# Kernel tuning notes

Measured on AMD Instinct MI355X. Metric: run time of the kernel, lower is better.

Reference implementation:

```python
import jax, jax.numpy as jnp
import numpy as np

CE_WEIGHT = 1.0
TRIPLET_WEIGHT = 0.1
MARGIN = 0.2


def setup_inputs() -> dict:
    key = jax.random.key(0)
    k1, k2, k3 = jax.random.split(key, 3)
    B, D, V = 4096, 512, 6000
    logits = jax.random.normal(k1, (B, V), dtype=jnp.float32)
    embeddings = jax.random.normal(k2, (B, D), dtype=jnp.float32)
    labels = jax.random.randint(k3, (B,), 0, 512, dtype=jnp.int64)
    return {"logits": logits, "embeddings": embeddings, "labels": labels}


def _pairwise_dist(emb):
    # Euclidean cdist via gram matrix; safe sqrt (zero grad where d2 == 0).
    sq = jnp.sum(emb * emb, axis=-1)  # [B]
    d2 = sq[:, None] + sq[None, :] - 2.0 * (emb @ emb.T)  # [B, B]
    d2 = jnp.maximum(d2, 0.0)
    safe = jnp.where(d2 > 0.0, d2, 1.0)
    return jnp.where(d2 > 0.0, jnp.sqrt(safe), 0.0)


def _losses(logits, embeddings, labels):
    B = logits.shape[0]
    # Cross entropy (mean reduction, matching nn.CrossEntropyLoss).
    logp = jax.nn.log_softmax(logits, axis=-1)
    ce_loss = -jnp.mean(jnp.take_along_axis(logp, labels[:, None], axis=1)[:, 0])

    # Batch-hard triplet loss, fully vectorized (one masked amax/amin per row).
    dist = _pairwise_dist(embeddings)  # [B, B]
    same = labels[:, None] == labels[None, :]  # [B, B]
    eye = jnp.eye(B, dtype=bool)
    pos_mask = same & ~eye
    neg_mask = ~same
    neg_inf = jnp.float32(-np.inf)
    pos_inf = jnp.float32(np.inf)
    hardest_pos = jnp.max(jnp.where(pos_mask, dist, neg_inf), axis=1)  # [B]
    hardest_neg = jnp.min(jnp.where(neg_mask, dist, pos_inf), axis=1)  # [B]
    valid = jnp.any(pos_mask, axis=1) & jnp.any(neg_mask, axis=1)  # [B]
    per_row = jax.nn.relu(hardest_pos - hardest_neg + MARGIN)
    per_row = jnp.where(valid, per_row, 0.0)
    n_valid = jnp.sum(valid.astype(jnp.float32))
    triplet_loss = jnp.where(n_valid > 0, jnp.sum(per_row) / jnp.maximum(n_valid, 1.0), 0.0)

    total_loss = CE_WEIGHT * ce_loss + TRIPLET_WEIGHT * triplet_loss
    return total_loss, ce_loss, triplet_loss


def reference(logits, embeddings, labels):
    return _losses(logits, embeddings, labels)
```

## Files before the change

### kernel.cpp

```cpp
#include <hip/hip_runtime.h>
#include <hip/hip_bf16.h>
#include <math.h>

#define BN   4096
#define DN   512
#define VN   6000
#define NCLS 512

typedef __attribute__((ext_vector_type(8)))  short short8;
typedef __attribute__((ext_vector_type(16))) float f32x16;

__device__ __forceinline__ unsigned short f2bf(float x) {
  unsigned int u = __float_as_uint(x);
  u = (u + 0x7FFFu + ((u >> 16) & 1u)) >> 16;
  return (unsigned short)u;
}

__device__ __forceinline__ void gld_lds16(const unsigned short* g, unsigned short* l) {
  __builtin_amdgcn_global_load_lds(
      (const __attribute__((address_space(1))) void*)g,
      (__attribute__((address_space(3))) void*)l, 16, 0, 0);
}

__launch_bounds__(256)
__global__ void prep_kernel(const float* __restrict__ emb, const int* __restrict__ labels,
                            unsigned short* __restrict__ embh, float* __restrict__ sqn,
                            int* __restrict__ cnt, int* __restrict__ posb,
                            int* __restrict__ negb) {
  const int row  = blockIdx.x * 4 + (threadIdx.x >> 6);
  const int lane = threadIdx.x & 63;
  const float4* rp = (const float4*)(emb + (size_t)row * DN);
  float4 a = rp[lane];
  float4 b = rp[lane + 64];
  float ss = a.x * a.x + a.y * a.y + a.z * a.z + a.w * a.w
           + b.x * b.x + b.y * b.y + b.z * b.z + b.w * b.w;
  ushort4 ha, hb;
  ha.x = f2bf(a.x); ha.y = f2bf(a.y); ha.z = f2bf(a.z); ha.w = f2bf(a.w);
  hb.x = f2bf(b.x); hb.y = f2bf(b.y); hb.z = f2bf(b.z); hb.w = f2bf(b.w);
  ushort4* wp = (ushort4*)(embh + (size_t)row * DN);
  wp[lane] = ha;
  wp[lane + 64] = hb;
#pragma unroll
  for (int off = 1; off < 64; off <<= 1) ss += __shfl_xor(ss, off);
  if (lane == 0) {
    sqn[row] = ss;
    posb[row] = 0;
    negb[row] = 0x7F800000;
    atomicAdd(cnt + labels[row], 1);
  }
}

__launch_bounds__(256)
__global__ void ce_kernel(const float* __restrict__ logits,
                          const int* __restrict__ labels,
                          float* __restrict__ ce_part) {
  const int r0 = blockIdx.x * 2, r1 = r0 + 1;
  const int tid = threadIdx.x;
  const float* p0 = logits + (size_t)r0 * VN;
  const float* p1 = logits + (size_t)r1 * VN;
  const float x0 = p0[labels[r0]];
  const float x1 = p1[labels[r1]];
  const float4* q0 = (const float4*)p0;
  const float4* q1 = (const float4*)p1;
  float4 v0[6], v1[6];
#pragma unroll
  for (int u = 0; u < 6; ++u) {
    int j = tid + u * 256;
    if (j < VN / 4) { v0[u] = q0[j]; v1[u] = q1[j]; }
  }
  float s0 = 0.f, s1 = 0.f;
#pragma unroll
  for (int u = 0; u < 6; ++u) {
    int j = tid + u * 256;
    if (j < VN / 4) {
      s0 += __expf(v0[u].x) + __expf(v0[u].y) + __expf(v0[u].z) + __expf(v0[u].w);
      s1 += __expf(v1[u].x) + __expf(v1[u].y) + __expf(v1[u].z) + __expf(v1[u].w);
    }
  }
#pragma unroll
  for (int off = 1; off < 64; off <<= 1) {
    s0 += __shfl_xor(s0, off);
    s1 += __shfl_xor(s1, off);
  }
  __shared__ float sp0[4], sp1[4];
  if ((tid & 63) == 0) { sp0[tid >> 6] = s0; sp1[tid >> 6] = s1; }
  __syncthreads();
  if (tid == 0) {
    ce_part[r0] = logf(sp0[0] + sp0[1] + sp0[2] + sp0[3]) - x0;
    ce_part[r1] = logf(sp1[0] + sp1[1] + sp1[2] + sp1[3]) - x1;
  }
}

__launch_bounds__(64, 2)
__global__ void triplet_kernel(const unsigned short* __restrict__ embh,
                               const float* __restrict__ sqn,
                               const int* __restrict__ labels,
                               int* __restrict__ posb, int* __restrict__ negb) {
  __shared__ unsigned short sA[64 * 64];
  __shared__ unsigned short sB[64 * 64];

  const int lane = threadIdx.x;
  const int m = lane & 31;
  const int half = lane >> 5;

  const int t = blockIdx.x;
  int J = (int)((sqrtf(8.f * (float)t + 1.f) - 1.f) * 0.5f);
  while ((J + 1) * (J + 2) / 2 <= t) ++J;
  while (J * (J + 1) / 2 > t) --J;
  const int I = t - J * (J + 1) / 2;
  const int i0 = I * 64, j0 = J * 64;
  const bool diag = (I == J);

  const int lrow = lane >> 3;
  const int lchk = (lane & 7) ^ lrow;
  const unsigned short* gA = embh + (size_t)(i0 + lrow) * DN + lchk * 8;
  const unsigned short* gB = embh + (size_t)(j0 + lrow) * DN + lchk * 8;

  f32x16 acc[2][2] = {};
  f32x16 accT[2][2] = {};

  for (int ks = 0; ks < 8; ++ks) {
    const int kk = ks * 64;
    asm volatile("s_waitcnt lgkmcnt(0)" ::: "memory");
#pragma unroll
    for (int s = 0; s < 8; ++s)
      gld_lds16(gA + kk + (size_t)s * 8 * DN, &sA[s * 8 * 64]);
#pragma unroll
    for (int s = 0; s < 8; ++s)
      gld_lds16(gB + kk + (size_t)s * 8 * DN, &sB[s * 8 * 64]);
    asm volatile("s_waitcnt vmcnt(0)" ::: "memory");
#pragma unroll
    for (int q = 0; q < 4; ++q) {
      const int c = q * 2 + half;
      const int sw = ((c ^ (m & 7)) * 8);
      short8 a0 = *(const short8*)&sA[m * 64 + sw];
      short8 a1 = *(const short8*)&sA[(32 + m) * 64 + sw];
      short8 b0 = *(const short8*)&sB[m * 64 + sw];
      short8 b1 = *(const short8*)&sB[(32 + m) * 64 + sw];
      acc[0][0]  = __builtin_amdgcn_mfma_f32_32x32x16_bf16(a0, b0, acc[0][0], 0, 0, 0);
      acc[0][1]  = __builtin_amdgcn_mfma_f32_32x32x16_bf16(a0, b1, acc[0][1], 0, 0, 0);
      acc[1][0]  = __builtin_amdgcn_mfma_f32_32x32x16_bf16(a1, b0, acc[1][0], 0, 0, 0);
      acc[1][1]  = __builtin_amdgcn_mfma_f32_32x32x16_bf16(a1, b1, acc[1][1], 0, 0, 0);
      accT[0][0] = __builtin_amdgcn_mfma_f32_32x32x16_bf16(b0, a0, accT[0][0], 0, 0, 0);
      accT[0][1] = __builtin_amdgcn_mfma_f32_32x32x16_bf16(b0, a1, accT[0][1], 0, 0, 0);
      accT[1][0] = __builtin_amdgcn_mfma_f32_32x32x16_bf16(b1, a0, accT[1][0], 0, 0, 0);
      accT[1][1] = __builtin_amdgcn_mfma_f32_32x32x16_bf16(b1, a1, accT[1][1], 0, 0, 0);
    }
  }

  {
    const int gj0 = j0 + m, gj1 = j0 + 32 + m;
    const int cl0 = labels[gj0], cl1 = labels[gj1];
    const float cq0 = sqn[gj0], cq1 = sqn[gj1];
    float p0 = 0.f, p1 = 0.f, n0 = INFINITY, n1 = INFINITY;
#pragma unroll
    for (int rb = 0; rb < 2; ++rb) {
#pragma unroll
      for (int r = 0; r < 16; ++r) {
        const int gi = i0 + rb * 32 + (r & 3) + 8 * (r >> 2) + 4 * half;
        const int rl = labels[gi];
        const float rq = sqn[gi];
        const float d0 = fmaf(-2.f, acc[rb][0][r], rq + cq0);
        const float d1 = fmaf(-2.f, acc[rb][1][r], rq + cq1);
        if (rl == cl0) { if (gi != gj0) p0 = fmaxf(p0, d0); } else n0 = fminf(n0, d0);
        if (rl == cl1) { if (gi != gj1) p1 = fmaxf(p1, d1); } else n1 = fminf(n1, d1);
      }
    }
    p0 = fmaxf(p0, __shfl_xor(p0, 32)); n0 = fminf(n0, __shfl_xor(n0, 32));
    p1 = fmaxf(p1, __shfl_xor(p1, 32)); n1 = fminf(n1, __shfl_xor(n1, 32));
    if (half == 0) {
      atomicMax(posb + gj0, __float_as_int(p0));
      atomicMin(negb + gj0, __float_as_int(n0));
      atomicMax(posb + gj1, __float_as_int(p1));
      atomicMin(negb + gj1, __float_as_int(n1));
    }
  }

  if (!diag) {
    const int gj0 = i0 + m, gj1 = i0 + 32 + m;
    const int cl0 = labels[gj0], cl1 = labels[gj1];
    const float cq0 = sqn[gj0], cq1 = sqn[gj1];
    float p0 = 0.f, p1 = 0.f, n0 = INFINITY, n1 = INFINITY;
#pragma unroll
    for (int rb = 0; rb < 2; ++rb) {
#pragma unroll
      for (int r = 0; r < 16; ++r) {
        const int gi = j0 + rb * 32 + (r & 3) + 8 * (r >> 2) + 4 * half;
        const int rl = labels[gi];
        const float rq = sqn[gi];
        const float d0 = fmaf(-2.f, accT[rb][0][r], rq + cq0);
        const float d1 = fmaf(-2.f, accT[rb][1][r], rq + cq1);
        if (rl == cl0) p0 = fmaxf(p0, d0); else n0 = fminf(n0, d0);
        if (rl == cl1) p1 = fmaxf(p1, d1); else n1 = fminf(n1, d1);
      }
    }
    p0 = fmaxf(p0, __shfl_xor(p0, 32)); n0 = fminf(n0, __shfl_xor(n0, 32));
    p1 = fmaxf(p1, __shfl_xor(p1, 32)); n1 = fminf(n1, __shfl_xor(n1, 32));
    if (half == 0) {
      atomicMax(posb + gj0, __float_as_int(p0));
      atomicMin(negb + gj0, __float_as_int(n0));
      atomicMax(posb + gj1, __float_as_int(p1));
      atomicMin(negb + gj1, __float_as_int(n1));
    }
  }
}

__launch_bounds__(1024)
__global__ void finalize_kernel(const int* __restrict__ posb, const int* __restrict__ negb,
                                const int* __restrict__ labels, const int* __restrict__ cnt,
                                const float* __restrict__ ce_part, float* __restrict__ out) {
  const int tid = threadIdx.x;
  float cesum = 0.f, sum = 0.f, nv = 0.f;
#pragma unroll
  for (int u = 0; u < 4; ++u) {
    const int i = tid + u * 1024;
    cesum += ce_part[i];
    int c = cnt[labels[i]];
    float p = sqrtf(fmaxf(__int_as_float(posb[i]), 0.f));
    float n = sqrtf(fmaxf(__int_as_float(negb[i]), 0.f));
    float t = fmaxf(p - n + 0.2f, 0.f);
    if (c >= 2 && c < BN) { sum += t; nv += 1.f; }
  }
#pragma unroll
  for (int off = 1; off < 64; off <<= 1) {
    cesum += __shfl_xor(cesum, off);
    sum   += __shfl_xor(sum, off);
    nv    += __shfl_xor(nv, off);
  }
  __shared__ float s0[16], s1[16], s2[16];
  if ((tid & 63) == 0) { s0[tid >> 6] = cesum; s1[tid >> 6] = sum; s2[tid >> 6] = nv; }
  __syncthreads();
  if (tid == 0) {
    cesum = 0.f; sum = 0.f; nv = 0.f;
#pragma unroll
    for (int wv = 0; wv < 16; ++wv) { cesum += s0[wv]; sum += s1[wv]; nv += s2[wv]; }
    float trip = (nv > 0.f) ? sum / nv : 0.f;
    float ce = cesum * (1.f / BN);
    out[0] = ce + 0.1f * trip;
    out[1] = ce;
    out[2] = trip;
  }
}

extern "C" void kernel_launch(void* const* d_in, const int* in_sizes, int n_in,
                              void* d_out, int out_size, void* d_ws, size_t ws_size,
                              hipStream_t stream) {
  const float* logits = (const float*)d_in[0];
  const float* emb    = (const float*)d_in[1];
  const int*   labels = (const int*)d_in[2];
  float* out = (float*)d_out;

  char* ws = (char*)d_ws;
  unsigned short* embh = (unsigned short*)ws;
  float* sqn    = (float*)(ws + (size_t)BN * DN * 2);
  int*   posb   = (int*)((char*)sqn  + (size_t)BN * 4);
  int*   negb   = (int*)((char*)posb + (size_t)BN * 4);
  int*   cnt    = (int*)((char*)negb + (size_t)BN * 4);
  float* ce_part = (float*)((char*)cnt + (size_t)NCLS * 4);

  hipMemsetAsync(cnt, 0, (size_t)NCLS * 4, stream);
  hipLaunchKernelGGL(prep_kernel, dim3(BN / 4), dim3(256), 0, stream,
                     emb, labels, embh, sqn, cnt, posb, negb);
  hipLaunchKernelGGL(ce_kernel, dim3(BN / 2), dim3(256), 0, stream,
                     logits, labels, ce_part);
  hipLaunchKernelGGL(triplet_kernel, dim3(64 * 65 / 2), dim3(64), 0, stream,
                     embh, sqn, labels, posb, negb);
  hipLaunchKernelGGL(finalize_kernel, dim3(1), dim3(1024), 0, stream,
                     posb, negb, labels, cnt, ce_part, out);
}
```

Before: 193.4 us.

## Fuse cross-entropy and triplet tiles into one interleaved kernel launch

Merges the memory-bound cross-entropy row reduction and the compute-bound triplet MFMA tiles into one heterogeneous kernel. Blocks are interleaved so each triplet tile is followed by two single-row CE blocks, letting logits streaming overlap with matrix work on the same CUs. The first 32 blocks take the leftover triplet tiles. This drops one launch and the serialization between the two kernels, but CE now runs with 64-thread blocks holding 24 float4 registers each, which may raise register pressure and reduce occupancy.

```diff
diff --git a/kernel.cpp b/kernel.cpp
--- a/kernel.cpp
+++ b/kernel.cpp
@@ -50,60 +50,15 @@
   }
 }
 
-__launch_bounds__(256)
-__global__ void ce_kernel(const float* __restrict__ logits,
-                          const int* __restrict__ labels,
-                          float* __restrict__ ce_part) {
-  const int r0 = blockIdx.x * 2, r1 = r0 + 1;
-  const int tid = threadIdx.x;
-  const float* p0 = logits + (size_t)r0 * VN;
-  const float* p1 = logits + (size_t)r1 * VN;
-  const float x0 = p0[labels[r0]];
-  const float x1 = p1[labels[r1]];
-  const float4* q0 = (const float4*)p0;
-  const float4* q1 = (const float4*)p1;
-  float4 v0[6], v1[6];
-#pragma unroll
-  for (int u = 0; u < 6; ++u) {
-    int j = tid + u * 256;
-    if (j < VN / 4) { v0[u] = q0[j]; v1[u] = q1[j]; }
-  }
-  float s0 = 0.f, s1 = 0.f;
-#pragma unroll
-  for (int u = 0; u < 6; ++u) {
-    int j = tid + u * 256;
-    if (j < VN / 4) {
-      s0 += __expf(v0[u].x) + __expf(v0[u].y) + __expf(v0[u].z) + __expf(v0[u].w);
-      s1 += __expf(v1[u].x) + __expf(v1[u].y) + __expf(v1[u].z) + __expf(v1[u].w);
-    }
-  }
-#pragma unroll
-  for (int off = 1; off < 64; off <<= 1) {
-    s0 += __shfl_xor(s0, off);
-    s1 += __shfl_xor(s1, off);
-  }
-  __shared__ float sp0[4], sp1[4];
-  if ((tid & 63) == 0) { sp0[tid >> 6] = s0; sp1[tid >> 6] = s1; }
-  __syncthreads();
-  if (tid == 0) {
-    ce_part[r0] = logf(sp0[0] + sp0[1] + sp0[2] + sp0[3]) - x0;
-    ce_part[r1] = logf(sp1[0] + sp1[1] + sp1[2] + sp1[3]) - x1;
-  }
-}
-
-__launch_bounds__(64, 2)
-__global__ void triplet_kernel(const unsigned short* __restrict__ embh,
-                               const float* __restrict__ sqn,
-                               const int* __restrict__ labels,
-                               int* __restrict__ posb, int* __restrict__ negb) {
-  __shared__ unsigned short sA[64 * 64];
-  __shared__ unsigned short sB[64 * 64];
-
-  const int lane = threadIdx.x;
+__device__ __forceinline__ void triplet_job(int t, unsigned short* sA, unsigned short* sB,
+                                            const unsigned short* __restrict__ embh,
+                                            const float* __restrict__ sqn,
+                                            const int* __restrict__ labels,
+                                            int* __restrict__ posb,
+                                            int* __restrict__ negb, int lane) {
   const int m = lane & 31;
   const int half = lane >> 5;
 
-  const int t = blockIdx.x;
   int J = (int)((sqrtf(8.f * (float)t + 1.f) - 1.f) * 0.5f);
   while ((J + 1) * (J + 2) / 2 <= t) ++J;
   while (J * (J + 1) / 2 > t) --J;
@@ -205,6 +160,49 @@
   }
 }
 
+__launch_bounds__(64, 2)
+__global__ void fused_kernel(const float* __restrict__ logits,
+                             const int* __restrict__ labels,
+                             float* __restrict__ ce_part,
+                             const unsigned short* __restrict__ embh,
+                             const float* __restrict__ sqn,
+                             int* __restrict__ posb, int* __restrict__ negb) {
+  __shared__ unsigned short smem[8192];
+  const int b = blockIdx.x;
+  const int lane = threadIdx.x;
+
+  int trip_job, ce_row;
+  if (b < 32) {
+    trip_job = 2048 + b; ce_row = -1;
+  } else {
+    const int g = (b - 32) / 3, r = (b - 32) % 3;
+    if (r == 0) { trip_job = g; ce_row = -1; }
+    else        { trip_job = -1; ce_row = g * 2 + (r - 1); }
+  }
+
+  if (trip_job >= 0) {
+    triplet_job(trip_job, smem, smem + 4096, embh, sqn, labels, posb, negb, lane);
+    return;
+  }
+
+  const float* rp = logits + (size_t)ce_row * VN;
+  const float xlab = rp[labels[ce_row]];
+  const float4* q = (const float4*)rp;
+  float4 v[24];
+#pragma unroll
+  for (int u = 0; u < 23; ++u) v[u] = q[lane + u * 64];
+  if (lane < 28) v[23] = q[lane + 23 * 64];
+  float s = 0.f;
+#pragma unroll
+  for (int u = 0; u < 23; ++u)
+    s += __expf(v[u].x) + __expf(v[u].y) + __expf(v[u].z) + __expf(v[u].w);
+  if (lane < 28)
+    s += __expf(v[23].x) + __expf(v[23].y) + __expf(v[23].z) + __expf(v[23].w);
+#pragma unroll
+  for (int off = 1; off < 64; off <<= 1) s += __shfl_xor(s, off);
+  if (lane == 0) ce_part[ce_row] = logf(s) - xlab;
+}
+
 __launch_bounds__(1024)
 __global__ void finalize_kernel(const int* __restrict__ posb, const int* __restrict__ negb,
                                 const int* __restrict__ labels, const int* __restrict__ cnt,
@@ -261,10 +259,8 @@
   hipMemsetAsync(cnt, 0, (size_t)NCLS * 4, stream);
   hipLaunchKernelGGL(prep_kernel, dim3(BN / 4), dim3(256), 0, stream,
                      emb, labels, embh, sqn, cnt, posb, negb);
-  hipLaunchKernelGGL(ce_kernel, dim3(BN / 2), dim3(256), 0, stream,
-                     logits, labels, ce_part);
-  hipLaunchKernelGGL(triplet_kernel, dim3(64 * 65 / 2), dim3(64), 0, stream,
-                     embh, sqn, labels, posb, negb);
+  hipLaunchKernelGGL(fused_kernel, dim3(32 + 2048 * 3), dim3(64), 0, stream,
+                     logits, labels, ce_part, embh, sqn, posb, negb);
   hipLaunchKernelGGL(finalize_kernel, dim3(1), dim3(1024), 0, stream,
                      posb, negb, labels, cnt, ce_part, out);
 }
```

After: 181.0 us. 6.4% less time.
